# Kernel tuning notes

Measured on AMD Instinct MI355X. Metric: run time of the kernel, lower is better.

Reference implementation:

```python
import jax, jax.numpy as jnp
import numpy as np

B = 64        # BATCH_SIZE
C_IN = 16
L = 8192
FFT0 = 64
FFT1 = 256
CO = 32       # c_out per fft branch (c_out=64 / 2 ffts)
RATIO = FFT1 // FFT0  # 4
EPS = 1e-5


def setup_inputs() -> dict:
    key = jax.random.key(0)
    ks = jax.random.split(key, 12)
    x = jax.random.normal(ks[0], (B, C_IN, L), jnp.float32)
    bn_gamma = 1.0 + 0.1 * jax.random.normal(ks[1], (2, B), jnp.float32)
    bn_beta = 0.1 * jax.random.normal(ks[2], (2, B), jnp.float32)
    mk_r = 0.1 * jax.random.normal(ks[3], (RATIO, RATIO), jnp.float32)
    mk_i = 0.1 * jax.random.normal(ks[4], (RATIO, RATIO), jnp.float32)
    mb_r = 0.1 * jax.random.normal(ks[5], (RATIO,), jnp.float32)
    mb_i = 0.1 * jax.random.normal(ks[6], (RATIO,), jnp.float32)
    fk0_r = 0.1 * jax.random.normal(ks[7], (FFT0 // 2 + 1, C_IN, CO), jnp.float32)
    fk0_i = 0.1 * jax.random.normal(ks[8], (FFT0 // 2 + 1, C_IN, CO), jnp.float32)
    fk1_r = 0.1 * jax.random.normal(ks[9], (FFT1 // 2 + 1, C_IN, CO), jnp.float32)
    fk1_i = 0.1 * jax.random.normal(ks[10], (FFT1 // 2 + 1, C_IN, CO), jnp.float32)
    pbias = 0.1 * jax.random.normal(ks[11], (2 * CO,), jnp.float32)
    return dict(x=x, bn_gamma=bn_gamma, bn_beta=bn_beta, mk_r=mk_r, mk_i=mk_i,
                mb_r=mb_r, mb_i=mb_i, fk0_r=fk0_r, fk0_i=fk0_i,
                fk1_r=fk1_r, fk1_i=fk1_i, pbias=pbias)


def _stft(x2d, n):
    # torch.stft(center=True, pad_mode='reflect', hop=n_fft, rect window),
    # then keep onesided bins and drop the last frame (as in the module).
    N = x2d.shape[0]
    xp = jnp.pad(x2d, ((0, 0), (n // 2, n // 2)), mode='reflect')
    frames = xp.reshape(N, -1, n)               # (N, T+1, n), hop == n_fft
    spec = jnp.fft.rfft(frames, axis=-1)        # onesided == [:, :, :n//2+1]
    return spec[:, :-1, :]                      # drop last frame -> (N, T, n//2+1)


def _zero_interp(p, ratio, out_f):
    # interleave (ratio-1) zeros along the freq axis, then crop to out_f bins
    b, t, f, c = p.shape
    z = jnp.zeros((b, t, f, ratio - 1, c), p.dtype)
    q = jnp.concatenate([p[:, :, :, None, :], z], axis=3).reshape(b, t, f * ratio, c)
    return q[:, :, :out_f, :]


def _cbn(xc, g, b):
    # BatchNorm2d(BATCH_SIZE) after permute(3,0,1,2): channel dim == batch dim,
    # stats over (c_in, T, F) per batch element; complex mean, |.|^2 variance.
    mu = jnp.mean(xc, axis=(1, 2, 3), keepdims=True)
    d = xc - mu
    var = jnp.mean((d * jnp.conj(d)).real, axis=(1, 2, 3), keepdims=True)
    xh = d / jnp.sqrt(var + EPS)
    return xh * g[:, None, None, None] + b[:, None, None, None]


def _istft(out, n):
    # out: (B, T, F, CO) complex. Mirrors permute/reshape + frame repeat + istft
    # (hop=n_fft, rect window, center=True -> trim n//2 on both ends).
    Bq, T, F, Co = out.shape
    pf = out.transpose(0, 3, 2, 1).reshape(Bq * Co, F, T)
    pf = jnp.concatenate([pf, pf[:, :, :1]], axis=-1)   # append copy of frame 0 -> T+1 frames
    fr = jnp.fft.irfft(pf, n=n, axis=1)                 # (N, n, T+1)
    sig = fr.transpose(0, 2, 1).reshape(Bq * Co, -1)    # overlap-add trivial (hop=n)
    sig = sig[:, n // 2: n // 2 + T * n]                # length L
    return sig.reshape(Bq, Co, -1).transpose(0, 2, 1)   # (B, L, CO)


def _forward(x, bn_gamma, bn_beta, mk_r, mk_i, mb_r, mb_i,
             fk0_r, fk0_i, fk1_r, fk1_i, pbias):
    x2 = x.reshape(B * C_IN, L)

    def spec(n):
        s = _stft(x2, n)                                 # (B*C_IN, T, n//2+1)
        T = s.shape[1]
        return s.reshape(B, C_IN, T, n // 2 + 1).transpose(0, 2, 3, 1)  # (B,T,F,C_IN)

    p0 = spec(FFT0)   # (B, 128, 33, 16)
    p1 = spec(FFT1)   # (B, 32, 129, 16)

    # attention merge across time (small fft -> large fft scale)
    pm = p0.reshape(B, -1, RATIO, FFT0 // 2 + 1, C_IN).transpose(0, 1, 3, 4, 2)  # (B,T1,F0,C,r)
    kc = mk_r + 1j * mk_i
    att = jnp.einsum('btfcr,rs->btfcs', pm, kc) + (mb_r + 1j * mb_i)
    a = jax.nn.softmax(jnp.abs(att), axis=-1)            # real weights (complex(a,0) in torch)
    merged = jnp.sum(pm * a, axis=-1) * float(RATIO)     # (B, T1, F0, C_IN)

    F1 = FFT1 // 2 + 1
    mask01 = _zero_interp(jnp.ones(merged.shape, jnp.float32), RATIO, F1)
    up = _zero_interp(merged, RATIO, F1)

    acc0 = p0                                            # own-scale mask is all ones
    acc1 = mask01 * up + (1.0 - mask01) * p1             # cross-scale + complementary mask

    def head(acc, g, b, fkr, fki, n):
        xbn = _cbn(acc, g, b)
        out = jnp.einsum('btfi,fio->btfo', xbn, fkr + 1j * fki)  # FILTER_FLAG merge
        return _istft(out, n)

    t0 = head(acc0, bn_gamma[0], bn_beta[0], fk0_r, fk0_i, FFT0)  # (B, L, CO)
    t1 = head(acc1, bn_gamma[1], bn_beta[1], fk1_r, fk1_i, FFT1)  # (B, L, CO)

    y = jnp.concatenate([t0, t1], axis=2) + pbias        # + patch_bias.real
    y = jax.nn.relu(y)                                   # ACT_DOMAIN == 'time'
    return y.transpose(0, 2, 1)                          # (B, c_out, L)


def reference(x, bn_gamma, bn_beta, mk_r, mk_i, mb_r, mb_i,
              fk0_r, fk0_i, fk1_r, fk1_i, pbias):
    return _forward(x, bn_gamma, bn_beta, mk_r, mk_i, mb_r, mb_i,
                    fk0_r, fk0_i, fk1_r, fk1_i, pbias)
```

## Files before the change

kernel.cpp:

```cpp
#include <hip/hip_runtime.h>
#include <math.h>

#define BB   64
#define CIN  16
#define LL   8192
#define CO   32
#define TCO  64
constexpr int T0n = 128;
constexpr int T1n = 32;
constexpr int F0n = 33;
constexpr int F1n = 129;

typedef unsigned int   uint32;
typedef unsigned short u16;
typedef __attribute__((ext_vector_type(8))) _Float16 half8;
typedef __attribute__((ext_vector_type(4))) float    f32x4;
typedef __attribute__((ext_vector_type(4))) uint32   u32x4;

__device__ inline half8 flip_pm(half8 v) {
    u32x4 u;
    __builtin_memcpy(&u, &v, 16);
    u.y ^= 0x80008000u;
    u.w ^= 0x80008000u;
    half8 r;
    __builtin_memcpy(&r, &u, 16);
    return r;
}

template<int N, int F, int TFR, int NTILES, int KTT, int MT_W, int NT_W,
         int NT_STRIDE, bool MT_SPLIT>
__global__ __launch_bounds__(256)
void stft_mfma_kernel(const float* __restrict__ x,
                      const u16* __restrict__ dhi, const u16* __restrict__ dlo,
                      float* __restrict__ p) {
    constexpr int PADN = N + 8;
    __shared__ __align__(16) u16 Xhi[TFR * PADN];
    __shared__ __align__(16) u16 Xlo[TFR * PADN];
    int bc = blockIdx.x;
    const float* xrow = x + (size_t)bc * LL;

    for (int i = threadIdx.x; i < TFR * N; i += 256) {
        int row = i / N, colk = i % N;
        int gi = i - N / 2;
        gi = gi < 0 ? -gi : gi;
        float v = xrow[gi];
        _Float16 h = (_Float16)v;
        _Float16 l = (_Float16)(v - (float)h);
        Xhi[row * PADN + colk] = *(u16*)&h;
        Xlo[row * PADN + colk] = *(u16*)&l;
    }
    __syncthreads();

    int lane = threadIdx.x & 63, w = threadIdx.x >> 6;
    int col = lane & 15, quad = lane >> 4;
    f32x4 acc[MT_W][NT_W];
    #pragma unroll
    for (int mi = 0; mi < MT_W; ++mi)
        #pragma unroll
        for (int nj = 0; nj < NT_W; ++nj) {
            f32x4 z = {0.f, 0.f, 0.f, 0.f};
            acc[mi][nj] = z;
        }

    for (int kt = 0; kt < KTT; ++kt) {
        half8 ah[MT_W], al[MT_W];
        #pragma unroll
        for (int mi = 0; mi < MT_W; ++mi) {
            int mt = MT_SPLIT ? (w * MT_W + mi) : mi;
            int t  = mt * 16 + col;
            ah[mi] = *(const half8*)&Xhi[t * PADN + kt * 32 + quad * 8];
            al[mi] = *(const half8*)&Xlo[t * PADN + kt * 32 + quad * 8];
        }
        #pragma unroll
        for (int nj = 0; nj < NT_W; ++nj) {
            int nt = MT_SPLIT ? nj : (w + nj * NT_STRIDE);
            if (nt < NTILES) {
                half8 bh = ((const half8*)dhi)[(nt * KTT + kt) * 64 + lane];
                half8 bl = ((const half8*)dlo)[(nt * KTT + kt) * 64 + lane];
                #pragma unroll
                for (int mi = 0; mi < MT_W; ++mi) {
                    acc[mi][nj] = __builtin_amdgcn_mfma_f32_16x16x32_f16(ah[mi], bh, acc[mi][nj], 0, 0, 0);
                    acc[mi][nj] = __builtin_amdgcn_mfma_f32_16x16x32_f16(ah[mi], bl, acc[mi][nj], 0, 0, 0);
                    acc[mi][nj] = __builtin_amdgcn_mfma_f32_16x16x32_f16(al[mi], bh, acc[mi][nj], 0, 0, 0);
                }
            }
        }
    }

    int b = bc / CIN, c = bc % CIN;
    #pragma unroll
    for (int mi = 0; mi < MT_W; ++mi) {
        int mt = MT_SPLIT ? (w * MT_W + mi) : mi;
        #pragma unroll
        for (int nj = 0; nj < NT_W; ++nj) {
            int nt = MT_SPLIT ? nj : (w + nj * NT_STRIDE);
            if (nt < NTILES) {
                int j = nt * 16 + col;
                if (j < 2 * F) {
                    int t0 = mt * 16 + quad * 4;
                    f32x4 a = acc[mi][nj];
                    #pragma unroll
                    for (int r = 0; r < 4; ++r) {
                        p[(((size_t)b * TFR + t0 + r) * CIN + c) * (2 * F) + j] = a[r];
                    }
                }
            }
        }
    }
}

__global__ __launch_bounds__(256)
void init_d_kernel(u16* __restrict__ dhi0, u16* __restrict__ dlo0,
                   u16* __restrict__ dhi1, u16* __restrict__ dlo1) {
    int idx = blockIdx.x * 256 + threadIdx.x;
    constexpr int SZ0 = 5 * 2 * 64 * 8;
    constexpr int SZ1 = 17 * 8 * 64 * 8;
    int N, F, KTT, id; u16 *dh, *dl;
    if (idx < SZ0)            { N = 64;  F = F0n; KTT = 2; dh = dhi0; dl = dlo0; id = idx; }
    else if (idx < SZ0 + SZ1) { N = 256; F = F1n; KTT = 8; dh = dhi1; dl = dlo1; id = idx - SZ0; }
    else return;
    int jj   = id & 7;
    int lane = (id >> 3) & 63;
    int rest = id >> 9;
    int kt   = rest % KTT;
    int nt   = rest / KTT;
    int j = nt * 16 + (lane & 15);
    int k = kt * 32 + (lane >> 4) * 8 + jj;
    float v = 0.f;
    if (j < 2 * F) {
        int f = j >> 1;
        int u = (f * k) % N;
        double th = 6.283185307179586476925286766559 * (double)u / (double)N;
        v = (float)((j & 1) ? -sin(th) : cos(th));
    }
    _Float16 h = (_Float16)v;
    _Float16 l = (_Float16)(v - (float)h);
    dh[id] = *(u16*)&h;
    dl[id] = *(u16*)&l;
}

__global__ __launch_bounds__(256)
void merge_kernel(const float2* __restrict__ p0, float2* __restrict__ p1,
                  const float* __restrict__ mkr, const float* __restrict__ mki,
                  const float* __restrict__ mbr, const float* __restrict__ mbi) {
    int idx = blockIdx.x * 256 + threadIdx.x;
    const int total = BB * T1n * CIN * F0n;
    if (idx >= total) return;
    int f0 = idx % F0n; int r1 = idx / F0n;
    int c  = r1 % CIN;  int r2 = r1 / CIN;
    int t1 = r2 % T1n;  int b  = r2 / T1n;
    float2 pm[4];
    #pragma unroll
    for (int r = 0; r < 4; ++r) {
        int t = t1 * 4 + r;
        pm[r] = p0[(((size_t)b * T0n + t) * CIN + c) * F0n + f0];
    }
    float mag[4], mx = -1e30f;
    #pragma unroll
    for (int s = 0; s < 4; ++s) {
        float atr = mbr[s], ati = mbi[s];
        #pragma unroll
        for (int r = 0; r < 4; ++r) {
            float kr = mkr[r * 4 + s], ki = mki[r * 4 + s];
            atr = fmaf(pm[r].x, kr, atr); atr = fmaf(-pm[r].y, ki, atr);
            ati = fmaf(pm[r].x, ki, ati); ati = fmaf(pm[r].y, kr, ati);
        }
        mag[s] = sqrtf(atr * atr + ati * ati);
        mx = fmaxf(mx, mag[s]);
    }
    float se = 0.f;
    #pragma unroll
    for (int s = 0; s < 4; ++s) { mag[s] = expf(mag[s] - mx); se += mag[s]; }
    float inv = 4.0f / se;
    float mr = 0.f, mi = 0.f;
    #pragma unroll
    for (int r = 0; r < 4; ++r) { mr = fmaf(pm[r].x, mag[r], mr); mi = fmaf(pm[r].y, mag[r], mi); }
    p1[(((size_t)b * T1n + t1) * CIN + c) * F1n + 4 * f0] = make_float2(mr * inv, mi * inv);
}

__global__ __launch_bounds__(256)
void cbn_kernel(const float2* __restrict__ p0, const float2* __restrict__ p1,
                const float* __restrict__ gamma, const float* __restrict__ beta,
                float4* __restrict__ bn) {
    int head = blockIdx.x >> 6;
    int b    = blockIdx.x & 63;
    int Nel  = head ? (T1n * CIN * F1n) : (T0n * CIN * F0n);
    const float2* base = head ? (p1 + (size_t)b * (T1n * CIN * F1n))
                              : (p0 + (size_t)b * (T0n * CIN * F0n));
    float sr = 0.f, si = 0.f, s2 = 0.f;
    for (int i = threadIdx.x; i < Nel; i += 256) {
        float2 v = base[i];
        sr += v.x; si += v.y;
        s2 = fmaf(v.x, v.x, s2); s2 = fmaf(v.y, v.y, s2);
    }
    __shared__ float red[3][256];
    red[0][threadIdx.x] = sr; red[1][threadIdx.x] = si; red[2][threadIdx.x] = s2;
    __syncthreads();
    for (int off = 128; off > 0; off >>= 1) {
        if (threadIdx.x < off) {
            red[0][threadIdx.x] += red[0][threadIdx.x + off];
            red[1][threadIdx.x] += red[1][threadIdx.x + off];
            red[2][threadIdx.x] += red[2][threadIdx.x + off];
        }
        __syncthreads();
    }
    if (threadIdx.x == 0) {
        float invN = 1.f / (float)Nel;
        float mur = red[0][0] * invN, mui = red[1][0] * invN;
        float var = red[2][0] * invN - mur * mur - mui * mui;
        float g = gamma[head * BB + b] * rsqrtf(var + 1e-5f);
        bn[head * BB + b] = make_float4(g, beta[head * BB + b] - mur * g, -mui * g, 0.f);
    }
}

__global__ __launch_bounds__(256)
void init_w_kernel(u16* __restrict__ whi0, u16* __restrict__ wlo0,
                   u16* __restrict__ whi1, u16* __restrict__ wlo1) {
    int idx = blockIdx.x * 256 + threadIdx.x;
    constexpr int SZ0 = 2 * 3 * 64 * 8;
    constexpr int SZ1 = 8 * 9 * 64 * 8;
    int N, F, KT, id; u16 *dh, *dl;
    if (idx < SZ0)            { N = 64;  F = F0n; KT = 3; dh = whi0; dl = wlo0; id = idx; }
    else if (idx < SZ0 + SZ1) { N = 256; F = F1n; KT = 9; dh = whi1; dl = wlo1; id = idx - SZ0; }
    else return;
    int j    = id & 7;
    int lane = (id >> 3) & 63;
    int rest = id >> 9;
    int kt   = rest % KT;
    int mt   = rest / KT;
    int m  = mt * 16 + (lane & 15);
    int k2 = kt * 32 + (lane >> 4) * 8 + j;
    float v = 0.f;
    if (k2 < 2 * F) {
        int f = k2 >> 1;
        double scale = (f == 0 || f == F - 1) ? (1024.0 / N) : (2048.0 / N);
        int u = (m * f) % N;
        double th = 6.283185307179586476925286766559 * (double)u / (double)N;
        v = (float)((k2 & 1) ? (-scale * sin(th)) : (scale * cos(th)));
    }
    _Float16 h = (_Float16)v;
    _Float16 l = (_Float16)(v - (float)h);
    dh[id] = *(u16*)&h;
    dl[id] = *(u16*)&l;
}

__global__ __launch_bounds__(256)
void init_fk_kernel(const float* __restrict__ r0, const float* __restrict__ i0,
                    const float* __restrict__ r1, const float* __restrict__ i1,
                    float4* __restrict__ q0, float4* __restrict__ q1,
                    float2* __restrict__ s0, float2* __restrict__ s1) {
    int idx = blockIdx.x * 256 + threadIdx.x;
    constexpr int NQ0 = 8 * F0n * 32;
    constexpr int NQ1 = 8 * F1n * 32;
    constexpr int NS0 = F0n * 32;
    constexpr int NS1 = F1n * 32;
    if (idx < NQ0) {
        int id = idx;
        int c2 = id / (F0n * 32); int rem = id % (F0n * 32);
        int f = rem >> 5, o = rem & 31;
        int s = (f * CIN + 2 * c2) * CO + o;
        q0[id] = make_float4(r0[s], i0[s], r0[s + CO], i0[s + CO]);
    } else if (idx < NQ0 + NQ1) {
        int id = idx - NQ0;
        int c2 = id / (F1n * 32); int rem = id % (F1n * 32);
        int f = rem >> 5, o = rem & 31;
        int s = (f * CIN + 2 * c2) * CO + o;
        q1[id] = make_float4(r1[s], i1[s], r1[s + CO], i1[s + CO]);
    } else if (idx < NQ0 + NQ1 + NS0) {
        int id = idx - NQ0 - NQ1;
        int f = id >> 5, o = id & 31;
        float sr = 0.f, si = 0.f;
        for (int ci = 0; ci < CIN; ++ci) {
            int s = (f * CIN + ci) * CO + o;
            sr += r0[s]; si += i0[s];
        }
        s0[id] = make_float2(sr, si);
    } else if (idx < NQ0 + NQ1 + NS0 + NS1) {
        int id = idx - NQ0 - NQ1 - NS0;
        int f = id >> 5, o = id & 31;
        float sr = 0.f, si = 0.f;
        for (int ci = 0; ci < CIN; ++ci) {
            int s = (f * CIN + ci) * CO + o;
            sr += r1[s]; si += i1[s];
        }
        s1[id] = make_float2(sr, si);
    }
}

template<int F, int TFR, int CH0, int G>
__global__ __launch_bounds__(256)
void einsum_kernel(const float2* __restrict__ p, const float4* __restrict__ fkq,
                   const float2* __restrict__ fks, const float4* __restrict__ bn,
                   float2* __restrict__ S) {
    constexpr int FCO = F * 32;
    constexpr int NG  = TFR / G;
    __shared__ float2 xs[G][CIN * F];
    int grp = blockIdx.x % NG, b = blockIdx.x / NG;
    float4 par = bn[(CH0 ? 1 : 0) * BB + b];
    {
        const float4* a4 = (const float4*)(p + ((size_t)b * TFR + grp * G) * CIN * F);
        float4* x4 = (float4*)&xs[0][0];
        for (int i = threadIdx.x; i < G * CIN * F / 2; i += 256) x4[i] = a4[i];
    }
    __syncthreads();
    float2* Sg = S + ((size_t)b * TFR + (size_t)grp * G) * FCO;
    for (int i = threadIdx.x; i < FCO; i += 256) {
        int f = i >> 5;
        float4 kk[8];
        #pragma unroll
        for (int c2 = 0; c2 < 8; ++c2) kk[c2] = fkq[c2 * FCO + i];
        float2 fv = fks[i];
        float base_re = fmaf(par.y, fv.x, -par.z * fv.y);
        float base_im = fmaf(par.y, fv.y,  par.z * fv.x);
        #pragma unroll 4
        for (int g = 0; g < G; ++g) {
            float re = 0.f, im = 0.f;
            #pragma unroll
            for (int c2 = 0; c2 < 8; ++c2) {
                float2 xa = xs[g][(2 * c2) * F + f];
                float2 xb = xs[g][(2 * c2 + 1) * F + f];
                float4 kkc = kk[c2];
                re = fmaf(xa.x, kkc.x, re); re = fmaf(-xa.y, kkc.y, re);
                im = fmaf(xa.x, kkc.y, im); im = fmaf(xa.y, kkc.x, im);
                re = fmaf(xb.x, kkc.z, re); re = fmaf(-xb.y, kkc.w, re);
                im = fmaf(xb.x, kkc.w, im); im = fmaf(xb.y, kkc.z, im);
            }
            Sg[(size_t)g * FCO + i] = make_float2(
                fmaf(par.x, re, base_re) * 32.f,
                fmaf(par.x, im, base_im) * 32.f);
        }
    }
}

template<int N, int F, int TFR, int CH0, int KT, int KPAD, int WBT, bool NTSPLIT>
__global__ __launch_bounds__(256)
void irfft_kernel(const float2* __restrict__ S,
                  const u16* __restrict__ whi, const u16* __restrict__ wlo,
                  const float* __restrict__ pbias, float* __restrict__ out) {
    constexpr int FCO = F * 32;
    constexpr int WNT = NTSPLIT ? 1 : 2;
    __shared__ __align__(16) u16 Shi[32][KPAD];
    __shared__ __align__(16) u16 Slo[32][KPAD];
    int t  = blockIdx.x % (TFR + 1);
    int b  = blockIdx.x / (TFR + 1);
    int tf = (t == TFR) ? 0 : t;
    const float2* src = S + ((size_t)b * TFR + tf) * FCO;
    for (int i = threadIdx.x; i < FCO; i += 256) {
        float2 v = src[i];
        int f = i >> 5, o = i & 31;
        _Float16 rh = (_Float16)v.x; _Float16 rl = (_Float16)(v.x - (float)rh);
        _Float16 ih = (_Float16)v.y; _Float16 il = (_Float16)(v.y - (float)ih);
        ((uint32*)&Shi[o][0])[f] = ((uint32)(*(u16*)&ih) << 16) | (uint32)(*(u16*)&rh);
        ((uint32*)&Slo[o][0])[f] = ((uint32)(*(u16*)&il) << 16) | (uint32)(*(u16*)&rl);
    }
    for (int i = threadIdx.x; i < 32 * (KT * 16 - F); i += 256) {
        constexpr int cols = KT * 16 - F;
        int o = i / cols, j = i - o * cols;
        ((uint32*)&Shi[o][0])[F + j] = 0;
        ((uint32*)&Slo[o][0])[F + j] = 0;
    }
    __syncthreads();

    int lane = threadIdx.x & 63, w = threadIdx.x >> 6;
    int col = lane & 15, quad = lane >> 4;
    f32x4 accB[WBT][WNT], accD[WBT][WNT];
    #pragma unroll
    for (int mi = 0; mi < WBT; ++mi)
        #pragma unroll
        for (int nj = 0; nj < WNT; ++nj) {
            f32x4 z = {0.f, 0.f, 0.f, 0.f};
            accB[mi][nj] = z; accD[mi][nj] = z;
        }
    for (int kt = 0; kt < KT; ++kt) {
        half8 bh[WNT], bl[WNT], bhm[WNT], blm[WNT];
        #pragma unroll
        for (int nj = 0; nj < WNT; ++nj) {
            int nt = NTSPLIT ? (w & 1) : nj;
            bh[nj]  = *(const half8*)&Shi[nt * 16 + col][kt * 32 + quad * 8];
            bl[nj]  = *(const half8*)&Slo[nt * 16 + col][kt * 32 + quad * 8];
            bhm[nj] = flip_pm(bh[nj]);
            blm[nj] = flip_pm(bl[nj]);
        }
        #pragma unroll
        for (int mi = 0; mi < WBT; ++mi) {
            int mt = NTSPLIT ? (w >> 1) : (w * WBT + mi);
            half8 ah = ((const half8*)whi)[(mt * KT + kt) * 64 + lane];
            half8 al = ((const half8*)wlo)[(mt * KT + kt) * 64 + lane];
            #pragma unroll
            for (int nj = 0; nj < WNT; ++nj) {
                accB[mi][nj] = __builtin_amdgcn_mfma_f32_16x16x32_f16(ah, bh[nj],  accB[mi][nj], 0, 0, 0);
                accB[mi][nj] = __builtin_amdgcn_mfma_f32_16x16x32_f16(ah, bl[nj],  accB[mi][nj], 0, 0, 0);
                accB[mi][nj] = __builtin_amdgcn_mfma_f32_16x16x32_f16(al, bh[nj],  accB[mi][nj], 0, 0, 0);
                accD[mi][nj] = __builtin_amdgcn_mfma_f32_16x16x32_f16(ah, bhm[nj], accD[mi][nj], 0, 0, 0);
                accD[mi][nj] = __builtin_amdgcn_mfma_f32_16x16x32_f16(ah, blm[nj], accD[mi][nj], 0, 0, 0);
                accD[mi][nj] = __builtin_amdgcn_mfma_f32_16x16x32_f16(al, bhm[nj], accD[mi][nj], 0, 0, 0);
            }
        }
    }
    constexpr float UNSCALE = 1.0f / 32768.0f;
    size_t bb = (size_t)b * TCO;
    #pragma unroll
    for (int mi = 0; mi < WBT; ++mi) {
        int mt = NTSPLIT ? (w >> 1) : (w * WBT + mi);
        #pragma unroll
        for (int hh = 0; hh < 2; ++hh) {
            int m  = mt * 16 + quad * 4 + hh * (N / 2);
            int l0 = t * N + m - N / 2;
            if ((unsigned)l0 < LL) {
                #pragma unroll
                for (int nj = 0; nj < WNT; ++nj) {
                    int nt = NTSPLIT ? (w & 1) : nj;
                    int ch = CH0 + nt * 16 + col;
                    float pb = pbias[ch];
                    f32x4 a = hh ? accD[mi][nj] : accB[mi][nj];
                    float4 v;
                    v.x = fmaxf(fmaf(a[0], UNSCALE, pb), 0.f);
                    v.y = fmaxf(fmaf(a[1], UNSCALE, pb), 0.f);
                    v.z = fmaxf(fmaf(a[2], UNSCALE, pb), 0.f);
                    v.w = fmaxf(fmaf(a[3], UNSCALE, pb), 0.f);
                    *(float4*)(out + (bb + ch) * LL + l0) = v;
                }
            }
        }
    }
}

extern "C" void kernel_launch(void* const* d_in, const int* in_sizes, int n_in,
                              void* d_out, int out_size, void* d_ws, size_t ws_size,
                              hipStream_t stream) {
    const float* x     = (const float*)d_in[0];
    const float* gam   = (const float*)d_in[1];
    const float* bet   = (const float*)d_in[2];
    const float* mkr   = (const float*)d_in[3];
    const float* mki   = (const float*)d_in[4];
    const float* mbr   = (const float*)d_in[5];
    const float* mbi   = (const float*)d_in[6];
    const float* fk0r  = (const float*)d_in[7];
    const float* fk0i  = (const float*)d_in[8];
    const float* fk1r  = (const float*)d_in[9];
    const float* fk1i  = (const float*)d_in[10];
    const float* pbias = (const float*)d_in[11];
    float* out = (float*)d_out;

    float2* p0   = (float2*)d_ws;
    float2* p1   = p0 + (size_t)BB * T0n * CIN * F0n;
    float4* bnp  = (float4*)(p1 + (size_t)BB * T1n * CIN * F1n);
    float4* fkq0 = bnp + 2 * BB;
    float4* fkq1 = fkq0 + 8 * F0n * 32;
    float2* fks0 = (float2*)(fkq1 + 8 * F1n * 32);
    float2* fks1 = fks0 + F0n * 32;
    float2* Sbuf = fks1 + F1n * 32;
    u16*    whi0 = (u16*)(Sbuf + (size_t)BB * T0n * F0n * 32);
    u16*    wlo0 = whi0 + 3072;
    u16*    whi1 = wlo0 + 3072;
    u16*    wlo1 = whi1 + 36864;
    u16*    dhi0 = wlo1 + 36864;
    u16*    dlo0 = dhi0 + 5120;
    u16*    dhi1 = dlo0 + 5120;
    u16*    dlo1 = dhi1 + 69632;

    init_w_kernel<<<(3072 + 36864 + 255) / 256, 256, 0, stream>>>(whi0, wlo0, whi1, wlo1);
    init_d_kernel<<<(5120 + 69632 + 255) / 256, 256, 0, stream>>>(dhi0, dlo0, dhi1, dlo1);
    init_fk_kernel<<<(8 * (F0n + F1n) * 32 + (F0n + F1n) * 32 + 255) / 256, 256, 0, stream>>>(
        fk0r, fk0i, fk1r, fk1i, fkq0, fkq1, fks0, fks1);
    stft_mfma_kernel<64, F0n, 128, 5, 2, 2, 5, 1, true><<<BB * CIN, 256, 0, stream>>>(
        x, dhi0, dlo0, (float*)p0);
    stft_mfma_kernel<256, F1n, 32, 17, 8, 2, 5, 4, false><<<BB * CIN, 256, 0, stream>>>(
        x, dhi1, dlo1, (float*)p1);
    merge_kernel<<<(BB * T1n * CIN * F0n) / 256, 256, 0, stream>>>(p0, p1, mkr, mki, mbr, mbi);
    cbn_kernel<<<128, 256, 0, stream>>>(p0, p1, gam, bet, bnp);
    einsum_kernel<F1n, T1n, 32, 4><<<BB * (T1n / 4), 256, 0, stream>>>(
        p1, fkq1, fks1, bnp, Sbuf);
    irfft_kernel<256, F1n, T1n, 32, 9, 296, 2, false><<<BB * (T1n + 1), 256, 0, stream>>>(
        Sbuf, whi1, wlo1, pbias, out);
    einsum_kernel<F0n, T0n, 0, 16><<<BB * (T0n / 16), 256, 0, stream>>>(
        p0, fkq0, fks0, bnp, Sbuf);
    irfft_kernel<64, F0n, T0n, 0, 3, 104, 1, true><<<BB * (T0n + 1), 256, 0, stream>>>(
        Sbuf, whi0, wlo0, pbias, out);
}
```

Before: 467.8 us.

## Split BN stats reduction, emit fp16 hi/lo spectra from einsum, pipeline irfft frames

The batch-norm statistics pass now runs as many partial-reduction blocks followed by a tiny finalize kernel, so it is no longer limited to 128 blocks. The einsum kernel writes its output already split into fp16 hi/lo pairs, in o-major padded rows that line up with the irfft MFMA tiles. This removes the per-block conversion and transpose that irfft used to do. Each irfft block now processes a run of frames and prefetches the next frame into registers while the current one computes, which lowers the block count and adds register pressure plus extra barriers.

```diff
diff --git a/kernel.cpp b/kernel.cpp
--- a/kernel.cpp
+++ b/kernel.cpp
@@ -16,6 +16,8 @@
 typedef __attribute__((ext_vector_type(8))) _Float16 half8;
 typedef __attribute__((ext_vector_type(4))) float    f32x4;
 typedef __attribute__((ext_vector_type(4))) uint32   u32x4;
+
+__device__ inline int imin(int a, int b) { return a < b ? a : b; }
 
 __device__ inline half8 flip_pm(half8 v) {
     u32x4 u;
@@ -179,16 +181,19 @@
 }
 
 __global__ __launch_bounds__(256)
-void cbn_kernel(const float2* __restrict__ p0, const float2* __restrict__ p1,
-                const float* __restrict__ gamma, const float* __restrict__ beta,
-                float4* __restrict__ bn) {
-    int head = blockIdx.x >> 6;
-    int b    = blockIdx.x & 63;
+void cbn_partial_kernel(const float2* __restrict__ p0, const float2* __restrict__ p1,
+                        float4* __restrict__ part) {
+    int blk  = blockIdx.x;
+    int c8   = blk & 7;
+    int b    = (blk >> 3) & 63;
+    int head = blk >> 9;
     int Nel  = head ? (T1n * CIN * F1n) : (T0n * CIN * F0n);
     const float2* base = head ? (p1 + (size_t)b * (T1n * CIN * F1n))
                               : (p0 + (size_t)b * (T0n * CIN * F0n));
+    int chunk = (Nel + 7) / 8;
+    int i0 = c8 * chunk, i1 = imin(i0 + chunk, Nel);
     float sr = 0.f, si = 0.f, s2 = 0.f;
-    for (int i = threadIdx.x; i < Nel; i += 256) {
+    for (int i = i0 + threadIdx.x; i < i1; i += 256) {
         float2 v = base[i];
         sr += v.x; si += v.y;
         s2 = fmaf(v.x, v.x, s2); s2 = fmaf(v.y, v.y, s2);
@@ -204,13 +209,28 @@
         }
         __syncthreads();
     }
-    if (threadIdx.x == 0) {
-        float invN = 1.f / (float)Nel;
-        float mur = red[0][0] * invN, mui = red[1][0] * invN;
-        float var = red[2][0] * invN - mur * mur - mui * mui;
-        float g = gamma[head * BB + b] * rsqrtf(var + 1e-5f);
-        bn[head * BB + b] = make_float4(g, beta[head * BB + b] - mur * g, -mui * g, 0.f);
-    }
+    if (threadIdx.x == 0)
+        part[blk] = make_float4(red[0][0], red[1][0], red[2][0], 0.f);
+}
+
+__global__ __launch_bounds__(128)
+void cbn_final_kernel(const float4* __restrict__ part,
+                      const float* __restrict__ gamma, const float* __restrict__ beta,
+                      float4* __restrict__ bn) {
+    int hb = threadIdx.x;
+    float sr = 0.f, si = 0.f, s2 = 0.f;
+    #pragma unroll
+    for (int c = 0; c < 8; ++c) {
+        float4 v = part[hb * 8 + c];
+        sr += v.x; si += v.y; s2 += v.z;
+    }
+    int head = hb >> 6;
+    int Nel  = head ? (T1n * CIN * F1n) : (T0n * CIN * F0n);
+    float invN = 1.f / (float)Nel;
+    float mur = sr * invN, mui = si * invN;
+    float var = s2 * invN - mur * mur - mui * mui;
+    float g = gamma[hb] * rsqrtf(var + 1e-5f);
+    bn[hb] = make_float4(g, beta[hb] - mur * g, -mui * g, 0.f);
 }
 
 __global__ __launch_bounds__(256)
@@ -257,18 +277,18 @@
     if (idx < NQ0) {
         int id = idx;
         int c2 = id / (F0n * 32); int rem = id % (F0n * 32);
-        int f = rem >> 5, o = rem & 31;
+        int o = rem / F0n, f = rem % F0n;
         int s = (f * CIN + 2 * c2) * CO + o;
         q0[id] = make_float4(r0[s], i0[s], r0[s + CO], i0[s + CO]);
     } else if (idx < NQ0 + NQ1) {
         int id = idx - NQ0;
         int c2 = id / (F1n * 32); int rem = id % (F1n * 32);
-        int f = rem >> 5, o = rem & 31;
+        int o = rem / F1n, f = rem % F1n;
         int s = (f * CIN + 2 * c2) * CO + o;
         q1[id] = make_float4(r1[s], i1[s], r1[s + CO], i1[s + CO]);
     } else if (idx < NQ0 + NQ1 + NS0) {
         int id = idx - NQ0 - NQ1;
-        int f = id >> 5, o = id & 31;
+        int o = id / F0n, f = id % F0n;
         float sr = 0.f, si = 0.f;
         for (int ci = 0; ci < CIN; ++ci) {
             int s = (f * CIN + ci) * CO + o;
@@ -277,7 +297,7 @@
         s0[id] = make_float2(sr, si);
     } else if (idx < NQ0 + NQ1 + NS0 + NS1) {
         int id = idx - NQ0 - NQ1 - NS0;
-        int f = id >> 5, o = id & 31;
+        int o = id / F1n, f = id % F1n;
         float sr = 0.f, si = 0.f;
         for (int ci = 0; ci < CIN; ++ci) {
             int s = (f * CIN + ci) * CO + o;
@@ -287,32 +307,32 @@
     }
 }
 
-template<int F, int TFR, int CH0, int G>
+template<int F, int TFR, int CH0, int G, int PADW>
 __global__ __launch_bounds__(256)
 void einsum_kernel(const float2* __restrict__ p, const float4* __restrict__ fkq,
                    const float2* __restrict__ fks, const float4* __restrict__ bn,
-                   float2* __restrict__ S) {
+                   uint32* __restrict__ Ghi, uint32* __restrict__ Glo) {
     constexpr int FCO = F * 32;
     constexpr int NG  = TFR / G;
     __shared__ float2 xs[G][CIN * F];
     int grp = blockIdx.x % NG, b = blockIdx.x / NG;
     float4 par = bn[(CH0 ? 1 : 0) * BB + b];
     {
-        const float4* a4 = (const float4*)(p + ((size_t)b * TFR + grp * G) * CIN * F);
+        const float4* a4 = (const float4*)(p + ((size_t)b * TFR + (size_t)grp * G) * CIN * F);
         float4* x4 = (float4*)&xs[0][0];
         for (int i = threadIdx.x; i < G * CIN * F / 2; i += 256) x4[i] = a4[i];
     }
     __syncthreads();
-    float2* Sg = S + ((size_t)b * TFR + (size_t)grp * G) * FCO;
+    size_t bt0 = (size_t)b * TFR + (size_t)grp * G;
     for (int i = threadIdx.x; i < FCO; i += 256) {
-        int f = i >> 5;
+        int o = i / F, f = i - o * F;
         float4 kk[8];
         #pragma unroll
         for (int c2 = 0; c2 < 8; ++c2) kk[c2] = fkq[c2 * FCO + i];
         float2 fv = fks[i];
         float base_re = fmaf(par.y, fv.x, -par.z * fv.y);
         float base_im = fmaf(par.y, fv.y,  par.z * fv.x);
-        #pragma unroll 4
+        #pragma unroll
         for (int g = 0; g < G; ++g) {
             float re = 0.f, im = 0.f;
             #pragma unroll
@@ -325,103 +345,140 @@
                 re = fmaf(xb.x, kkc.z, re); re = fmaf(-xb.y, kkc.w, re);
                 im = fmaf(xb.x, kkc.w, im); im = fmaf(xb.y, kkc.z, im);
             }
-            Sg[(size_t)g * FCO + i] = make_float2(
-                fmaf(par.x, re, base_re) * 32.f,
-                fmaf(par.x, im, base_im) * 32.f);
-        }
-    }
-}
-
-template<int N, int F, int TFR, int CH0, int KT, int KPAD, int WBT, bool NTSPLIT>
-__global__ __launch_bounds__(256)
-void irfft_kernel(const float2* __restrict__ S,
+            float res = fmaf(par.x, re, base_re) * 32.f;
+            float ims = fmaf(par.x, im, base_im) * 32.f;
+            _Float16 rh = (_Float16)res; _Float16 rl = (_Float16)(res - (float)rh);
+            _Float16 ih = (_Float16)ims; _Float16 il = (_Float16)(ims - (float)ih);
+            size_t d = ((bt0 + g) * 32 + o) * PADW + f;
+            Ghi[d] = ((uint32)(*(u16*)&ih) << 16) | (uint32)(*(u16*)&rh);
+            Glo[d] = ((uint32)(*(u16*)&il) << 16) | (uint32)(*(u16*)&rl);
+        }
+    }
+    constexpr int PADC = PADW - F;
+    for (int j = threadIdx.x; j < G * 32 * PADC; j += 256) {
+        int g = j / (32 * PADC); int r = j - g * (32 * PADC);
+        int o = r / PADC;        int c = r - o * PADC;
+        size_t d = ((bt0 + g) * 32 + o) * PADW + F + c;
+        Ghi[d] = 0; Glo[d] = 0;
+    }
+}
+
+template<int N, int F, int TFR, int CH0, int KT, int FRC, int WMT, bool NTSPLIT>
+__global__ __launch_bounds__(256)
+void irfft_kernel(const uint32* __restrict__ Ghi, const uint32* __restrict__ Glo,
                   const u16* __restrict__ whi, const u16* __restrict__ wlo,
                   const float* __restrict__ pbias, float* __restrict__ out) {
-    constexpr int FCO = F * 32;
-    constexpr int WNT = NTSPLIT ? 1 : 2;
-    __shared__ __align__(16) u16 Shi[32][KPAD];
-    __shared__ __align__(16) u16 Slo[32][KPAD];
-    int t  = blockIdx.x % (TFR + 1);
-    int b  = blockIdx.x / (TFR + 1);
-    int tf = (t == TFR) ? 0 : t;
-    const float2* src = S + ((size_t)b * TFR + tf) * FCO;
-    for (int i = threadIdx.x; i < FCO; i += 256) {
-        float2 v = src[i];
-        int f = i >> 5, o = i & 31;
-        _Float16 rh = (_Float16)v.x; _Float16 rl = (_Float16)(v.x - (float)rh);
-        _Float16 ih = (_Float16)v.y; _Float16 il = (_Float16)(v.y - (float)ih);
-        ((uint32*)&Shi[o][0])[f] = ((uint32)(*(u16*)&ih) << 16) | (uint32)(*(u16*)&rh);
-        ((uint32*)&Slo[o][0])[f] = ((uint32)(*(u16*)&il) << 16) | (uint32)(*(u16*)&rl);
-    }
-    for (int i = threadIdx.x; i < 32 * (KT * 16 - F); i += 256) {
-        constexpr int cols = KT * 16 - F;
-        int o = i / cols, j = i - o * cols;
-        ((uint32*)&Shi[o][0])[F + j] = 0;
-        ((uint32*)&Slo[o][0])[F + j] = 0;
-    }
-    __syncthreads();
-
+    constexpr int PADW = KT * 16;
+    constexpr int LDW  = PADW + 4;
+    constexpr int RW4  = PADW / 4;
+    constexpr int NLD  = (32 * RW4 + 255) / 256;
+    constexpr int NCH  = (TFR + 1 + FRC - 1) / FRC;
+    constexpr int WNT  = NTSPLIT ? 1 : 2;
+    __shared__ __align__(16) uint32 buf[2][32 * LDW];
+
+    int ch = blockIdx.x % NCH, b = blockIdx.x / NCH;
+    int ft0 = ch * FRC, ftend = imin(ft0 + FRC, TFR + 1);
     int lane = threadIdx.x & 63, w = threadIdx.x >> 6;
     int col = lane & 15, quad = lane >> 4;
-    f32x4 accB[WBT][WNT], accD[WBT][WNT];
-    #pragma unroll
-    for (int mi = 0; mi < WBT; ++mi)
-        #pragma unroll
-        for (int nj = 0; nj < WNT; ++nj) {
-            f32x4 z = {0.f, 0.f, 0.f, 0.f};
-            accB[mi][nj] = z; accD[mi][nj] = z;
-        }
-    for (int kt = 0; kt < KT; ++kt) {
-        half8 bh[WNT], bl[WNT], bhm[WNT], blm[WNT];
-        #pragma unroll
-        for (int nj = 0; nj < WNT; ++nj) {
-            int nt = NTSPLIT ? (w & 1) : nj;
-            bh[nj]  = *(const half8*)&Shi[nt * 16 + col][kt * 32 + quad * 8];
-            bl[nj]  = *(const half8*)&Slo[nt * 16 + col][kt * 32 + quad * 8];
-            bhm[nj] = flip_pm(bh[nj]);
-            blm[nj] = flip_pm(bl[nj]);
-        }
-        #pragma unroll
-        for (int mi = 0; mi < WBT; ++mi) {
-            int mt = NTSPLIT ? (w >> 1) : (w * WBT + mi);
-            half8 ah = ((const half8*)whi)[(mt * KT + kt) * 64 + lane];
-            half8 al = ((const half8*)wlo)[(mt * KT + kt) * 64 + lane];
+
+    float4 rh[NLD], rl[NLD];
+    auto stage_load = [&](int ft) {
+        int tf = (ft == TFR) ? 0 : ft;
+        const float4* sH = (const float4*)(Ghi + ((size_t)b * TFR + tf) * 32 * PADW);
+        const float4* sL = (const float4*)(Glo + ((size_t)b * TFR + tf) * 32 * PADW);
+        #pragma unroll
+        for (int q = 0; q < NLD; ++q) {
+            int i = threadIdx.x + q * 256;
+            if (i < 32 * RW4) { rh[q] = sH[i]; rl[q] = sL[i]; }
+        }
+    };
+    auto stage_write = [&]() {
+        #pragma unroll
+        for (int q = 0; q < NLD; ++q) {
+            int i = threadIdx.x + q * 256;
+            if (i < 32 * RW4) {
+                int row = i / RW4, c = i - row * RW4;
+                *(float4*)&buf[0][row * LDW + 4 * c] = rh[q];
+                *(float4*)&buf[1][row * LDW + 4 * c] = rl[q];
+            }
+        }
+    };
+
+    stage_load(ft0);
+    stage_write();
+    __syncthreads();
+
+    const u16* bufh = (const u16*)&buf[0][0];
+    const u16* bufl = (const u16*)&buf[1][0];
+    constexpr float UNSCALE = 1.0f / 32768.0f;
+    size_t bb = (size_t)b * TCO;
+
+    for (int ft = ft0; ft < ftend; ++ft) {
+        bool nxt = (ft + 1 < ftend);
+        if (nxt) stage_load(ft + 1);
+
+        f32x4 accB[WMT][WNT], accD[WMT][WNT];
+        #pragma unroll
+        for (int mi = 0; mi < WMT; ++mi)
             #pragma unroll
             for (int nj = 0; nj < WNT; ++nj) {
-                accB[mi][nj] = __builtin_amdgcn_mfma_f32_16x16x32_f16(ah, bh[nj],  accB[mi][nj], 0, 0, 0);
-                accB[mi][nj] = __builtin_amdgcn_mfma_f32_16x16x32_f16(ah, bl[nj],  accB[mi][nj], 0, 0, 0);
-                accB[mi][nj] = __builtin_amdgcn_mfma_f32_16x16x32_f16(al, bh[nj],  accB[mi][nj], 0, 0, 0);
-                accD[mi][nj] = __builtin_amdgcn_mfma_f32_16x16x32_f16(ah, bhm[nj], accD[mi][nj], 0, 0, 0);
-                accD[mi][nj] = __builtin_amdgcn_mfma_f32_16x16x32_f16(ah, blm[nj], accD[mi][nj], 0, 0, 0);
-                accD[mi][nj] = __builtin_amdgcn_mfma_f32_16x16x32_f16(al, bhm[nj], accD[mi][nj], 0, 0, 0);
-            }
-        }
-    }
-    constexpr float UNSCALE = 1.0f / 32768.0f;
-    size_t bb = (size_t)b * TCO;
-    #pragma unroll
-    for (int mi = 0; mi < WBT; ++mi) {
-        int mt = NTSPLIT ? (w >> 1) : (w * WBT + mi);
-        #pragma unroll
-        for (int hh = 0; hh < 2; ++hh) {
-            int m  = mt * 16 + quad * 4 + hh * (N / 2);
-            int l0 = t * N + m - N / 2;
-            if ((unsigned)l0 < LL) {
+                f32x4 z = {0.f, 0.f, 0.f, 0.f};
+                accB[mi][nj] = z; accD[mi][nj] = z;
+            }
+        for (int kt = 0; kt < KT; ++kt) {
+            half8 bh[WNT], bl[WNT], bhm[WNT], blm[WNT];
+            #pragma unroll
+            for (int nj = 0; nj < WNT; ++nj) {
+                int nt = NTSPLIT ? (w & 1) : nj;
+                int ro = (nt * 16 + col) * (2 * LDW) + kt * 32 + quad * 8;
+                bh[nj]  = *(const half8*)(bufh + ro);
+                bl[nj]  = *(const half8*)(bufl + ro);
+                bhm[nj] = flip_pm(bh[nj]);
+                blm[nj] = flip_pm(bl[nj]);
+            }
+            #pragma unroll
+            for (int mi = 0; mi < WMT; ++mi) {
+                int mt = NTSPLIT ? (w >> 1) : (w * WMT + mi);
+                half8 ah = ((const half8*)whi)[(mt * KT + kt) * 64 + lane];
+                half8 al = ((const half8*)wlo)[(mt * KT + kt) * 64 + lane];
                 #pragma unroll
                 for (int nj = 0; nj < WNT; ++nj) {
-                    int nt = NTSPLIT ? (w & 1) : nj;
-                    int ch = CH0 + nt * 16 + col;
-                    float pb = pbias[ch];
-                    f32x4 a = hh ? accD[mi][nj] : accB[mi][nj];
-                    float4 v;
-                    v.x = fmaxf(fmaf(a[0], UNSCALE, pb), 0.f);
-                    v.y = fmaxf(fmaf(a[1], UNSCALE, pb), 0.f);
-                    v.z = fmaxf(fmaf(a[2], UNSCALE, pb), 0.f);
-                    v.w = fmaxf(fmaf(a[3], UNSCALE, pb), 0.f);
-                    *(float4*)(out + (bb + ch) * LL + l0) = v;
+                    accB[mi][nj] = __builtin_amdgcn_mfma_f32_16x16x32_f16(ah, bh[nj],  accB[mi][nj], 0, 0, 0);
+                    accB[mi][nj] = __builtin_amdgcn_mfma_f32_16x16x32_f16(ah, bl[nj],  accB[mi][nj], 0, 0, 0);
+                    accB[mi][nj] = __builtin_amdgcn_mfma_f32_16x16x32_f16(al, bh[nj],  accB[mi][nj], 0, 0, 0);
+                    accD[mi][nj] = __builtin_amdgcn_mfma_f32_16x16x32_f16(ah, bhm[nj], accD[mi][nj], 0, 0, 0);
+                    accD[mi][nj] = __builtin_amdgcn_mfma_f32_16x16x32_f16(ah, blm[nj], accD[mi][nj], 0, 0, 0);
+                    accD[mi][nj] = __builtin_amdgcn_mfma_f32_16x16x32_f16(al, bhm[nj], accD[mi][nj], 0, 0, 0);
                 }
             }
         }
+        #pragma unroll
+        for (int mi = 0; mi < WMT; ++mi) {
+            int mt = NTSPLIT ? (w >> 1) : (w * WMT + mi);
+            #pragma unroll
+            for (int hh = 0; hh < 2; ++hh) {
+                int m  = mt * 16 + quad * 4 + hh * (N / 2);
+                int l0 = ft * N + m - N / 2;
+                if ((unsigned)l0 < LL) {
+                    #pragma unroll
+                    for (int nj = 0; nj < WNT; ++nj) {
+                        int nt = NTSPLIT ? (w & 1) : nj;
+                        int chn = CH0 + nt * 16 + col;
+                        float pb = pbias[chn];
+                        f32x4 a = hh ? accD[mi][nj] : accB[mi][nj];
+                        float4 v;
+                        v.x = fmaxf(fmaf(a[0], UNSCALE, pb), 0.f);
+                        v.y = fmaxf(fmaf(a[1], UNSCALE, pb), 0.f);
+                        v.z = fmaxf(fmaf(a[2], UNSCALE, pb), 0.f);
+                        v.w = fmaxf(fmaf(a[3], UNSCALE, pb), 0.f);
+                        *(float4*)(out + (bb + chn) * LL + l0) = v;
+                    }
+                }
+            }
+        }
+        __syncthreads();
+        if (nxt) stage_write();
+        __syncthreads();
     }
 }
 
@@ -445,12 +502,14 @@
     float2* p0   = (float2*)d_ws;
     float2* p1   = p0 + (size_t)BB * T0n * CIN * F0n;
     float4* bnp  = (float4*)(p1 + (size_t)BB * T1n * CIN * F1n);
-    float4* fkq0 = bnp + 2 * BB;
+    float4* part = bnp + 2 * BB;
+    float4* fkq0 = part + 1024;
     float4* fkq1 = fkq0 + 8 * F0n * 32;
     float2* fks0 = (float2*)(fkq1 + 8 * F1n * 32);
     float2* fks1 = fks0 + F0n * 32;
-    float2* Sbuf = fks1 + F1n * 32;
-    u16*    whi0 = (u16*)(Sbuf + (size_t)BB * T0n * F0n * 32);
+    uint32* Ghi  = (uint32*)(fks1 + F1n * 32);
+    uint32* Glo  = Ghi + (size_t)8192 * 32 * 48;
+    u16*    whi0 = (u16*)(Glo + (size_t)8192 * 32 * 48);
     u16*    wlo0 = whi0 + 3072;
     u16*    whi1 = wlo0 + 3072;
     u16*    wlo1 = whi1 + 36864;
@@ -468,13 +527,14 @@
     stft_mfma_kernel<256, F1n, 32, 17, 8, 2, 5, 4, false><<<BB * CIN, 256, 0, stream>>>(
         x, dhi1, dlo1, (float*)p1);
     merge_kernel<<<(BB * T1n * CIN * F0n) / 256, 256, 0, stream>>>(p0, p1, mkr, mki, mbr, mbi);
-    cbn_kernel<<<128, 256, 0, stream>>>(p0, p1, gam, bet, bnp);
-    einsum_kernel<F1n, T1n, 32, 4><<<BB * (T1n / 4), 256, 0, stream>>>(
-        p1, fkq1, fks1, bnp, Sbuf);
-    irfft_kernel<256, F1n, T1n, 32, 9, 296, 2, false><<<BB * (T1n + 1), 256, 0, stream>>>(
-        Sbuf, whi1, wlo1, pbias, out);
-    einsum_kernel<F0n, T0n, 0, 16><<<BB * (T0n / 16), 256, 0, stream>>>(
-        p0, fkq0, fks0, bnp, Sbuf);
-    irfft_kernel<64, F0n, T0n, 0, 3, 104, 1, true><<<BB * (T0n + 1), 256, 0, stream>>>(
-        Sbuf, whi0, wlo0, pbias, out);
-}
+    cbn_partial_kernel<<<1024, 256, 0, stream>>>(p0, p1, part);
+    cbn_final_kernel<<<1, 128, 0, stream>>>(part, gam, bet, bnp);
+    einsum_kernel<F1n, T1n, 32, 4, 144><<<BB * (T1n / 4), 256, 0, stream>>>(
+        p1, fkq1, fks1, bnp, Ghi, Glo);
+    irfft_kernel<256, F1n, T1n, 32, 9, 9, 2, false><<<BB * 4, 256, 0, stream>>>(
+        Ghi, Glo, whi1, wlo1, pbias, out);
+    einsum_kernel<F0n, T0n, 0, 8, 48><<<BB * (T0n / 8), 256, 0, stream>>>(
+        p0, fkq0, fks0, bnp, Ghi, Glo);
+    irfft_kernel<64, F0n, T0n, 0, 3, 17, 1, true><<<BB * 8, 256, 0, stream>>>(
+        Ghi, Glo, whi0, wlo0, pbias, out);
+}
```

Measured after the change: 517.6 us. 1.11x slower.
